# Kernel optimization log

Measured on AMD Instinct MI355X. Metric: run time of the kernel, lower is better.

Reference implementation:

```python
import jax, jax.numpy as jnp
import numpy as np

N_NODES = 40000
N_EDGES = 640000
IN_FEATS = 128
HID = 64
# layer widths per GCN.__init__: in->h->2h->2h->h->h->h->1
DIMS = [IN_FEATS, HID, 2 * HID, 2 * HID, HID, HID, HID, 1]


def setup_inputs() -> dict:
    key = jax.random.key(0)
    ks = jax.random.split(key, 3 + 2 * 7)
    inp = {
        "in_feat": jax.random.normal(ks[0], (N_NODES, IN_FEATS), dtype=jnp.float32),
        "src": jax.random.randint(ks[1], (N_EDGES,), 0, N_NODES, dtype=jnp.int32),
        "dst": jax.random.randint(ks[2], (N_EDGES,), 0, N_NODES, dtype=jnp.int32),
    }
    # DGL GraphConv params: weight [in, out] (glorot), bias [out] (zeros; use small randn for a nontrivial baseline)
    for i in range(7):
        din, dout = DIMS[i], DIMS[i + 1]
        scale = jnp.sqrt(6.0 / (din + dout)).astype(jnp.float32)
        inp[f"W{i+1}"] = jax.random.uniform(ks[3 + 2 * i], (din, dout), jnp.float32, -scale, scale)
        inp[f"b{i+1}"] = 0.01 * jax.random.normal(ks[4 + 2 * i], (dout,), dtype=jnp.float32)
    return inp


def _graph_conv(x, W, b, src, dst, out_norm, in_norm, n_nodes):
    # DGL GraphConv, norm='both', allow_zero_in_degree=True:
    #   h = D_in^{-1/2} * A^T * (D_out^{-1/2} * x) @ W + b
    x = x * out_norm[:, None]
    if x.shape[1] > W.shape[1]:
        # mult W first to shrink message dim (mirrors DGL's heuristic; math-equivalent)
        x = x @ W
        h = jax.ops.segment_sum(x[src], dst, num_segments=n_nodes)
    else:
        h = jax.ops.segment_sum(x[src], dst, num_segments=n_nodes)
        h = h @ W
    return h * in_norm[:, None] + b


def reference(in_feat, src, dst, W1, b1, W2, b2, W3, b3, W4, b4, W5, b5, W6, b6, W7, b7):
    n = in_feat.shape[0]
    ones = jnp.ones((src.shape[0],), dtype=jnp.float32)
    out_deg = jax.ops.segment_sum(ones, src, num_segments=n)
    in_deg = jax.ops.segment_sum(ones, dst, num_segments=n)
    out_norm = jnp.where(out_deg > 0, jax.lax.rsqrt(jnp.maximum(out_deg, 1.0)), 0.0)
    in_norm = jnp.where(in_deg > 0, jax.lax.rsqrt(jnp.maximum(in_deg, 1.0)), 0.0)

    params = [(W1, b1), (W2, b2), (W3, b3), (W4, b4), (W5, b5), (W6, b6), (W7, b7)]
    h = in_feat
    for i, (W, b) in enumerate(params):
        h = _graph_conv(h, W, b, src, dst, out_norm, in_norm, n)
        if i < 6:
            h = jax.nn.relu(h)
    return h  # [N, 1]
```

## Files before the change

kernel.cpp:

```cpp
#include <hip/hip_runtime.h>
#include <hip/hip_bf16.h>


#define IN_F 128
#define NSLICE 60
#define SHB 13
#define NSHARD 5

typedef __attribute__((ext_vector_type(8))) short short8v;
typedef __attribute__((ext_vector_type(4))) float f32x4;
typedef __attribute__((ext_vector_type(8))) _Float16 half8v;

static __device__ __forceinline__ unsigned short f2bf(float x) {
    unsigned u = __builtin_bit_cast(unsigned, x);
    unsigned r = (u + 0x7FFFu + ((u >> 16) & 1u)) >> 16;
    return (unsigned short)r;
}
static __device__ __forceinline__ float bf2f(unsigned short h) {
    unsigned u = ((unsigned)h) << 16;
    return __builtin_bit_cast(float, u);
}


__global__ __launch_bounds__(256) void hist2_kernel(const int* __restrict__ src,
                                                    const int* __restrict__ dst,
                                                    int* __restrict__ scratch, int E) {
    constexpr int SH = 1 << SHB;
    __shared__ int h[SH];
    const int t = threadIdx.x;
    const int b = blockIdx.x;
    const int s = blockIdx.y;
    const int z = blockIdx.z;
    const int* idx = z ? dst : src;
    for (int i = t; i < SH; i += 256) h[i] = 0;
    __syncthreads();
    const int per = (E + NSLICE - 1) / NSLICE;
    const int lo = b * per;
    const int hiE = min(lo + per, E);
    const int base = s << SHB;
    for (int e = lo + t; e < hiE; e += 256) {
        unsigned a = (unsigned)(idx[e] - base);
        if (a < (unsigned)SH) atomicAdd(&h[a], 1);
    }
    __syncthreads();
    int* so = scratch + ((size_t)((z * NSHARD + s) * NSLICE + b) << SHB);
    for (int i = t; i < SH; i += 256) so[i] = h[i];
}

__global__ void hist_reduce_kernel(const int* __restrict__ scratch,
                                   int* __restrict__ in_deg,
                                   float* __restrict__ out_nrm,
                                   float* __restrict__ in_nrm, int N) {
    constexpr int SH = 1 << SHB;
    int n = blockIdx.x * blockDim.x + threadIdx.x;
    if (n >= N) return;
    int s = n >> SHB;
    int i = n & (SH - 1);
    int od = 0, idg = 0;
    for (int b = 0; b < NSLICE; ++b) {
        od  += scratch[((size_t)((0 * NSHARD + s) * NSLICE + b) << SHB) + i];
        idg += scratch[((size_t)((1 * NSHARD + s) * NSLICE + b) << SHB) + i];
    }
    in_deg[n] = idg;
    out_nrm[n] = od  > 0 ? rsqrtf((float)od)  : 0.f;
    in_nrm[n]  = idg > 0 ? rsqrtf((float)idg) : 0.f;
}


__global__ __launch_bounds__(256) void scan_blk_kernel(const int* __restrict__ deg,
                                                       int* __restrict__ blockSums, int N) {
    __shared__ int ws[4];
    const int t = threadIdx.x;
    const int base = blockIdx.x * 1024 + t * 4;
    int4 v = make_int4(0, 0, 0, 0);
    if (base + 3 < N) v = *reinterpret_cast<const int4*>(&deg[base]);
    else if (base < N) {
        v.x = deg[base];
        if (base + 1 < N) v.y = deg[base + 1];
        if (base + 2 < N) v.z = deg[base + 2];
    }
    int s = v.x + v.y + v.z + v.w;
#pragma unroll
    for (int off = 32; off > 0; off >>= 1) s += __shfl_down(s, off);
    if ((t & 63) == 0) ws[t >> 6] = s;
    __syncthreads();
    if (t == 0) blockSums[blockIdx.x] = ws[0] + ws[1] + ws[2] + ws[3];
}

__global__ __launch_bounds__(64) void scan_top_kernel(const int* __restrict__ blockSums,
                                                      int* __restrict__ blockOffs,
                                                      int* __restrict__ row_off, int NB, int N) {
    const int t = threadIdx.x;
    int orig = (t < NB) ? blockSums[t] : 0;
    int v = orig;
#pragma unroll
    for (int off = 1; off < 64; off <<= 1) {
        int u = __shfl_up(v, off);
        if (t >= off) v += u;
    }
    if (t < NB) blockOffs[t] = v - orig;
    if (t == 63) row_off[N] = v;
}

__global__ __launch_bounds__(256) void scan_fill_kernel(const int* __restrict__ deg,
                                                        const int* __restrict__ blockOffs,
                                                        int* __restrict__ row_off,
                                                        int* __restrict__ cursor, int N) {
    __shared__ int wtot[4];
    const int t = threadIdx.x;
    const int lane = t & 63;
    const int wid = t >> 6;
    const int base = blockIdx.x * 1024 + t * 4;
    int4 v = make_int4(0, 0, 0, 0);
    if (base + 3 < N) v = *reinterpret_cast<const int4*>(&deg[base]);
    else if (base < N) {
        v.x = deg[base];
        if (base + 1 < N) v.y = deg[base + 1];
        if (base + 2 < N) v.z = deg[base + 2];
    }
    const int s = v.x + v.y + v.z + v.w;
    int incl = s;
#pragma unroll
    for (int off = 1; off < 64; off <<= 1) {
        int u = __shfl_up(incl, off);
        if (lane >= off) incl += u;
    }
    if (lane == 63) wtot[wid] = incl;
    __syncthreads();
    int pre = blockOffs[blockIdx.x] + incl - s;
    for (int i = 0; i < wid; ++i) pre += wtot[i];
    if (base < N) {
        int run = pre;
        row_off[base] = run; cursor[base] = run; run += v.x;
        if (base + 1 < N) { row_off[base + 1] = run; cursor[base + 1] = run; run += v.y; }
        if (base + 2 < N) { row_off[base + 2] = run; cursor[base + 2] = run; run += v.z; }
        if (base + 3 < N) { row_off[base + 3] = run; cursor[base + 3] = run; }
    }
}

__global__ void fill_kernel(const int* __restrict__ src, const int* __restrict__ dst,
                            int* __restrict__ cursor, int* __restrict__ csr, int E) {
    int e = blockIdx.x * blockDim.x + threadIdx.x;
    if (e < E) {
        int pos = atomicAdd(&cursor[dst[e]], 1);
        csr[pos] = src[e];
    }
}


__global__ void split_feat_kernel(const float* __restrict__ x, const float* __restrict__ snrm,
                                  unsigned short* __restrict__ th, unsigned short* __restrict__ tl,
                                  int total4) {
    int i = blockIdx.x * blockDim.x + threadIdx.x;
    if (i >= total4) return;
    float4 v = reinterpret_cast<const float4*>(x)[i];
    float sc = snrm[i >> 5];
    ushort4 h, l;
    float a;
    a = v.x * sc; h.x = f2bf(a); l.x = f2bf(a - bf2f(h.x));
    a = v.y * sc; h.y = f2bf(a); l.y = f2bf(a - bf2f(h.y));
    a = v.z * sc; h.z = f2bf(a); l.z = f2bf(a - bf2f(h.z));
    a = v.w * sc; h.w = f2bf(a); l.w = f2bf(a - bf2f(h.w));
    reinterpret_cast<ushort4*>(th)[i] = h;
    reinterpret_cast<ushort4*>(tl)[i] = l;
}

struct WDesc { const float* w; unsigned short* th; unsigned short* tl; int K; int N; };
struct WPack { WDesc d[6]; };

__global__ void split_w_kernel(WPack p) {
    WDesc d = p.d[blockIdx.x];
    int total = d.K * d.N;
    for (int i = threadIdx.x; i < total; i += blockDim.x) {
        int k = i / d.N, n = i - k * d.N;
        float v = d.w[i];
        unsigned short h = f2bf(v);
        d.th[(size_t)n * d.K + k] = h;
        d.tl[(size_t)n * d.K + k] = f2bf(v - bf2f(h));
    }
}


template<int K, int NOUT, bool POST, bool RELU, bool POST2, int OUTM>
__global__ __launch_bounds__(256) void gemm_mfma(
    const unsigned short* __restrict__ Ah, const unsigned short* __restrict__ Al,
    const unsigned short* __restrict__ Bh, const unsigned short* __restrict__ Bl,
    const float* __restrict__ r_nrm, const float* __restrict__ s_nrm,
    const float* __restrict__ bias,
    _Float16* __restrict__ Y16, unsigned short* __restrict__ Yh,
    unsigned short* __restrict__ Yl, int M) {
    constexpr int NT = NOUT / 16;
    const int lane = threadIdx.x & 63;
    const int wv = threadIdx.x >> 6;
    const int r0 = blockIdx.x * 64 + wv * 16;
    const int arow = r0 + (lane & 15);
    const int kg = (lane >> 4) * 8;

    f32x4 acc[NT];
#pragma unroll
    for (int n = 0; n < NT; ++n) acc[n] = (f32x4){0.f, 0.f, 0.f, 0.f};

    for (int kk = 0; kk < K; kk += 32) {
        short8v a_h = *reinterpret_cast<const short8v*>(Ah + (size_t)arow * K + kk + kg);
        short8v a_l = *reinterpret_cast<const short8v*>(Al + (size_t)arow * K + kk + kg);
#pragma unroll
        for (int n = 0; n < NT; ++n) {
            int col = n * 16 + (lane & 15);
            short8v b_h = *reinterpret_cast<const short8v*>(Bh + (size_t)col * K + kk + kg);
            short8v b_l = *reinterpret_cast<const short8v*>(Bl + (size_t)col * K + kk + kg);
            acc[n] = __builtin_amdgcn_mfma_f32_16x16x32_bf16(a_h, b_h, acc[n], 0, 0, 0);
            acc[n] = __builtin_amdgcn_mfma_f32_16x16x32_bf16(a_h, b_l, acc[n], 0, 0, 0);
            acc[n] = __builtin_amdgcn_mfma_f32_16x16x32_bf16(a_l, b_h, acc[n], 0, 0, 0);
        }
    }

    const int c0 = lane & 15;
    const int rr = r0 + (lane >> 4) * 4;
#pragma unroll
    for (int n = 0; n < NT; ++n) {
        const int col = n * 16 + c0;
        const float bcol = POST ? bias[col] : 0.f;
#pragma unroll
        for (int j = 0; j < 4; ++j) {
            const int row = rr + j;
            float y = acc[n][j];
            if (POST) y = fmaf(y, r_nrm[row], bcol);
            if (RELU) y = fmaxf(y, 0.f);
            if (POST2) y *= s_nrm[row];
            if (OUTM == 0) {
                Y16[(size_t)row * NOUT + col] = (_Float16)y;
            } else {
                unsigned short h = f2bf(y);
                Yh[(size_t)row * NOUT + col] = h;
                Yl[(size_t)row * NOUT + col] = f2bf(y - bf2f(h));
            }
        }
    }
}


template<int F, bool POST, bool RELU, bool POST2, int OUTM>
__global__ __launch_bounds__(256) void agg_h16(
    const _Float16* __restrict__ X, const int* __restrict__ csr,
    const int* __restrict__ row_off, const float* __restrict__ r_nrm,
    const float* __restrict__ s_nrm, const float* __restrict__ bias,
    _Float16* __restrict__ Y16, unsigned short* __restrict__ Yh,
    unsigned short* __restrict__ Yl, int N) {
    constexpr int LPE = F / 8;
    constexpr int EPW = 64 / LPE;
    const int lane = threadIdx.x & 63;
    const int node = blockIdx.x * (blockDim.x >> 6) + (threadIdx.x >> 6);
    if (node >= N) return;
    const int g = lane / LPE;
    const int c = lane % LPE;
    const int lo = row_off[node];
    const int hi = row_off[node + 1];
    float acc[8];
#pragma unroll
    for (int j = 0; j < 8; ++j) acc[j] = 0.f;
    for (int e = lo + g; e < hi; e += EPW) {
        int s = csr[e];
        half8v x = *reinterpret_cast<const half8v*>(&X[(size_t)s * F + c * 8]);
#pragma unroll
        for (int j = 0; j < 8; ++j) acc[j] += (float)x[j];
    }
#pragma unroll
    for (int m = LPE; m < 64; m <<= 1) {
#pragma unroll
        for (int j = 0; j < 8; ++j) acc[j] += __shfl_xor(acc[j], m);
    }
    if (lane < LPE) {
        if (POST) {
            float rn = r_nrm[node];
#pragma unroll
            for (int j = 0; j < 8; ++j) acc[j] = fmaf(acc[j], rn, bias[lane * 8 + j]);
        }
        if (RELU) {
#pragma unroll
            for (int j = 0; j < 8; ++j) acc[j] = fmaxf(acc[j], 0.f);
        }
        if (POST2) {
            float sn = s_nrm[node];
#pragma unroll
            for (int j = 0; j < 8; ++j) acc[j] *= sn;
        }
        if (OUTM == 0) {
            half8v o;
#pragma unroll
            for (int j = 0; j < 8; ++j) o[j] = (_Float16)acc[j];
            *reinterpret_cast<half8v*>(&Y16[(size_t)node * F + lane * 8]) = o;
        } else {
            short8v h, l;
#pragma unroll
            for (int j = 0; j < 8; ++j) {
                unsigned short hh = f2bf(acc[j]);
                h[j] = (short)hh;
                l[j] = (short)f2bf(acc[j] - bf2f(hh));
            }
            *reinterpret_cast<short8v*>(&Yh[(size_t)node * F + lane * 8]) = h;
            *reinterpret_cast<short8v*>(&Yl[(size_t)node * F + lane * 8]) = l;
        }
    }
}


__global__ __launch_bounds__(256) void gemv64_kernel(const _Float16* __restrict__ X,
                                                     const float* __restrict__ W,
                                                     float* __restrict__ Y, int M) {
    const int lane = threadIdx.x & 63;
    const int m = blockIdx.x * (blockDim.x >> 6) + (threadIdx.x >> 6);
    if (m >= M) return;
    float v = (float)X[(size_t)m * 64 + lane] * W[lane];
#pragma unroll
    for (int off = 32; off > 0; off >>= 1) v += __shfl_down(v, off);
    if (lane == 0) Y[m] = v;
}

__global__ __launch_bounds__(256) void agg1_kernel(const float* __restrict__ T,
                                                   const int* __restrict__ csr,
                                                   const int* __restrict__ row_off,
                                                   const float* __restrict__ r_nrm,
                                                   const float* __restrict__ bias,
                                                   float* __restrict__ Y, int N) {
    const int node = blockIdx.x * 16 + (threadIdx.x >> 4);
    const int l = threadIdx.x & 15;
    if (node >= N) return;
    const int lo = row_off[node];
    const int hi = row_off[node + 1];
    float acc = 0.f;
    for (int e = lo + l; e < hi; e += 16) acc += T[csr[e]];
#pragma unroll
    for (int m = 8; m >= 1; m >>= 1) acc += __shfl_xor(acc, m);
    if (l == 0) Y[node] = fmaf(acc, r_nrm[node], bias[0]);
}


extern "C" void kernel_launch(void* const* d_in, const int* in_sizes, int n_in,
                              void* d_out, int out_size, void* d_ws, size_t ws_size,
                              hipStream_t stream) {
    const float* in_feat = (const float*)d_in[0];
    const int* src = (const int*)d_in[1];
    const int* dst = (const int*)d_in[2];
    const float* W1 = (const float*)d_in[3];  const float* B1 = (const float*)d_in[4];
    const float* W2 = (const float*)d_in[5];  const float* B2 = (const float*)d_in[6];
    const float* W3 = (const float*)d_in[7];  const float* B3 = (const float*)d_in[8];
    const float* W4 = (const float*)d_in[9];  const float* B4 = (const float*)d_in[10];
    const float* W5 = (const float*)d_in[11]; const float* B5 = (const float*)d_in[12];
    const float* W6 = (const float*)d_in[13]; const float* B6 = (const float*)d_in[14];
    const float* W7 = (const float*)d_in[15]; const float* B7 = (const float*)d_in[16];

    const int N = in_sizes[0] / IN_F;
    const int E = in_sizes[1];
    float* out = (float*)d_out;

    char* w = (char*)d_ws;
    auto alloc = [&](size_t bytes) { char* p = w; w += (bytes + 255) & ~(size_t)255; return p; };
    int* csr      = (int*)alloc((size_t)E * 4);
    int* row_off  = (int*)alloc((size_t)(N + 1) * 4);
    int* cursor   = (int*)alloc((size_t)N * 4);
    int* in_deg   = (int*)alloc((size_t)N * 4);
    int* blockSums= (int*)alloc(64 * 4);
    int* blockOffs= (int*)alloc(64 * 4);
    float* out_nrm= (float*)alloc((size_t)N * 4);
    float* in_nrm = (float*)alloc((size_t)N * 4);
    float* t7     = (float*)alloc((size_t)N * 4);
    const int dims[8] = {128, 64, 128, 128, 64, 64, 64, 1};
    unsigned short* wth[6]; unsigned short* wtl[6];
    for (int i = 0; i < 6; ++i) {
        size_t kn = (size_t)dims[i] * dims[i + 1];
        wth[i] = (unsigned short*)alloc(kn * 2);
        wtl[i] = (unsigned short*)alloc(kn * 2);
    }
    unsigned short* fh = (unsigned short*)alloc((size_t)N * 128 * 2);
    unsigned short* fl = (unsigned short*)alloc((size_t)N * 128 * 2);
    unsigned short* th = (unsigned short*)alloc((size_t)N * 128 * 2);
    unsigned short* tl = (unsigned short*)alloc((size_t)N * 128 * 2);
    _Float16* h0 = (_Float16*)alloc((size_t)N * 128 * 2);
    _Float16* h1 = (_Float16*)alloc((size_t)N * 128 * 2);
    int* scratch = (int*)fh;
    (void)ws_size; (void)n_in; (void)out_size;

    const int TB = 256;
    const int NB = (N + 1023) / 1024;

    WPack wp;
    const float* Ws[6] = {W1, W2, W3, W4, W5, W6};
    for (int i = 0; i < 6; ++i) wp.d[i] = {Ws[i], wth[i], wtl[i], dims[i], dims[i + 1]};
    split_w_kernel<<<6, TB, 0, stream>>>(wp);

    hist2_kernel<<<dim3(NSLICE, NSHARD, 2), TB, 0, stream>>>(src, dst, scratch, E);
    hist_reduce_kernel<<<(N + TB - 1) / TB, TB, 0, stream>>>(
        scratch, in_deg, out_nrm, in_nrm, N);
    scan_blk_kernel<<<NB, TB, 0, stream>>>(in_deg, blockSums, N);
    scan_top_kernel<<<1, 64, 0, stream>>>(blockSums, blockOffs, row_off, NB, N);
    scan_fill_kernel<<<NB, TB, 0, stream>>>(in_deg, blockOffs, row_off, cursor, N);
    fill_kernel<<<(E + TB - 1) / TB, TB, 0, stream>>>(src, dst, cursor, csr, E);

    split_feat_kernel<<<(N * 32 + TB - 1) / TB, TB, 0, stream>>>(
        in_feat, out_nrm, fh, fl, N * 32);

    const int gridN4 = (N + 3) / 4;
    const int MB = N / 64;

    gemm_mfma<128, 64, false, false, false, 0><<<MB, TB, 0, stream>>>(
        fh, fl, wth[0], wtl[0], nullptr, nullptr, nullptr, h0, nullptr, nullptr, N);
    agg_h16<64, true, true, true, 0><<<gridN4, TB, 0, stream>>>(
        h0, csr, row_off, in_nrm, out_nrm, B1, h1, nullptr, nullptr, N);

    agg_h16<64, false, false, false, 1><<<gridN4, TB, 0, stream>>>(
        h1, csr, row_off, nullptr, nullptr, nullptr, nullptr, th, tl, N);
    gemm_mfma<64, 128, true, true, true, 0><<<MB, TB, 0, stream>>>(
        th, tl, wth[1], wtl[1], in_nrm, out_nrm, B2, h0, nullptr, nullptr, N);

    agg_h16<128, false, false, false, 1><<<gridN4, TB, 0, stream>>>(
        h0, csr, row_off, nullptr, nullptr, nullptr, nullptr, th, tl, N);
    gemm_mfma<128, 128, true, true, true, 1><<<MB, TB, 0, stream>>>(
        th, tl, wth[2], wtl[2], in_nrm, out_nrm, B3, nullptr, fh, fl, N);

    gemm_mfma<128, 64, false, false, false, 0><<<MB, TB, 0, stream>>>(
        fh, fl, wth[3], wtl[3], nullptr, nullptr, nullptr, h0, nullptr, nullptr, N);
    agg_h16<64, true, true, true, 0><<<gridN4, TB, 0, stream>>>(
        h0, csr, row_off, in_nrm, out_nrm, B4, h1, nullptr, nullptr, N);

    agg_h16<64, false, false, false, 1><<<gridN4, TB, 0, stream>>>(
        h1, csr, row_off, nullptr, nullptr, nullptr, nullptr, th, tl, N);
    gemm_mfma<64, 64, true, true, true, 0><<<MB, TB, 0, stream>>>(
        th, tl, wth[4], wtl[4], in_nrm, out_nrm, B5, h0, nullptr, nullptr, N);

    agg_h16<64, false, false, false, 1><<<gridN4, TB, 0, stream>>>(
        h0, csr, row_off, nullptr, nullptr, nullptr, nullptr, th, tl, N);
    gemm_mfma<64, 64, true, true, true, 0><<<MB, TB, 0, stream>>>(
        th, tl, wth[5], wtl[5], in_nrm, out_nrm, B6, h1, nullptr, nullptr, N);

    gemv64_kernel<<<gridN4, TB, 0, stream>>>(h1, W7, t7, N);
    agg1_kernel<<<(N + 15) / 16, TB, 0, stream>>>(t7, csr, row_off, in_nrm, B7, out, N);
}
```

Measured before the change: 343.8 us.

## Build CSR with per-slice LDS cursors from histogram; unroll aggregation; parallelize weight split

Result: faster. 310.2 us (-9.8%).

```diff
diff --git a/kernel.cpp b/kernel.cpp
--- a/kernel.cpp
+++ b/kernel.cpp
@@ -104,8 +104,7 @@
 
 __global__ __launch_bounds__(256) void scan_fill_kernel(const int* __restrict__ deg,
                                                         const int* __restrict__ blockOffs,
-                                                        int* __restrict__ row_off,
-                                                        int* __restrict__ cursor, int N) {
+                                                        int* __restrict__ row_off, int N) {
     __shared__ int wtot[4];
     const int t = threadIdx.x;
     const int lane = t & 63;
@@ -131,19 +130,51 @@
     for (int i = 0; i < wid; ++i) pre += wtot[i];
     if (base < N) {
         int run = pre;
-        row_off[base] = run; cursor[base] = run; run += v.x;
-        if (base + 1 < N) { row_off[base + 1] = run; cursor[base + 1] = run; run += v.y; }
-        if (base + 2 < N) { row_off[base + 2] = run; cursor[base + 2] = run; run += v.z; }
-        if (base + 3 < N) { row_off[base + 3] = run; cursor[base + 3] = run; }
-    }
-}
-
-__global__ void fill_kernel(const int* __restrict__ src, const int* __restrict__ dst,
-                            int* __restrict__ cursor, int* __restrict__ csr, int E) {
-    int e = blockIdx.x * blockDim.x + threadIdx.x;
-    if (e < E) {
-        int pos = atomicAdd(&cursor[dst[e]], 1);
-        csr[pos] = src[e];
+        row_off[base] = run; run += v.x;
+        if (base + 1 < N) { row_off[base + 1] = run; run += v.y; }
+        if (base + 2 < N) { row_off[base + 2] = run; run += v.z; }
+        if (base + 3 < N) { row_off[base + 3] = run; }
+    }
+}
+
+__global__ void slice_base_kernel(int* __restrict__ scratch,
+                                  const int* __restrict__ row_off, int N) {
+    constexpr int SH = 1 << SHB;
+    int n = blockIdx.x * blockDim.x + threadIdx.x;
+    if (n >= N) return;
+    int s = n >> SHB;
+    int i = n & (SH - 1);
+    int run = row_off[n];
+    for (int b = 0; b < NSLICE; ++b) {
+        size_t off = ((size_t)((NSHARD + s) * NSLICE + b) << SHB) + i;
+        int c = scratch[off];
+        scratch[off] = run;
+        run += c;
+    }
+}
+
+__global__ __launch_bounds__(256) void fill2_kernel(const int* __restrict__ src,
+                                                    const int* __restrict__ dst,
+                                                    const int* __restrict__ scratch,
+                                                    int* __restrict__ csr, int E) {
+    constexpr int SH = 1 << SHB;
+    __shared__ int cur[SH];
+    const int t = threadIdx.x;
+    const int b = blockIdx.x;
+    const int s = blockIdx.y;
+    const int* base = scratch + ((size_t)((NSHARD + s) * NSLICE + b) << SHB);
+    for (int i = t; i < SH; i += 256) cur[i] = base[i];
+    __syncthreads();
+    const int per = (E + NSLICE - 1) / NSLICE;
+    const int lo = b * per;
+    const int hiE = min(lo + per, E);
+    const int nb = s << SHB;
+    for (int e = lo + t; e < hiE; e += 256) {
+        unsigned a = (unsigned)(dst[e] - nb);
+        if (a < (unsigned)SH) {
+            int pos = atomicAdd(&cur[a], 1);
+            csr[pos] = src[e];
+        }
     }
 }
 
@@ -168,16 +199,15 @@
 struct WDesc { const float* w; unsigned short* th; unsigned short* tl; int K; int N; };
 struct WPack { WDesc d[6]; };
 
-__global__ void split_w_kernel(WPack p) {
+__global__ __launch_bounds__(256) void split_w_kernel(WPack p) {
     WDesc d = p.d[blockIdx.x];
-    int total = d.K * d.N;
-    for (int i = threadIdx.x; i < total; i += blockDim.x) {
-        int k = i / d.N, n = i - k * d.N;
-        float v = d.w[i];
-        unsigned short h = f2bf(v);
-        d.th[(size_t)n * d.K + k] = h;
-        d.tl[(size_t)n * d.K + k] = f2bf(v - bf2f(h));
-    }
+    int i = blockIdx.y * 256 + threadIdx.x;
+    if (i >= d.K * d.N) return;
+    int k = i / d.N, n = i - k * d.N;
+    float v = d.w[i];
+    unsigned short h = f2bf(v);
+    d.th[(size_t)n * d.K + k] = h;
+    d.tl[(size_t)n * d.K + k] = f2bf(v - bf2f(h));
 }
 
 
@@ -255,15 +285,26 @@
     const int c = lane % LPE;
     const int lo = row_off[node];
     const int hi = row_off[node + 1];
-    float acc[8];
-#pragma unroll
-    for (int j = 0; j < 8; ++j) acc[j] = 0.f;
-    for (int e = lo + g; e < hi; e += EPW) {
-        int s = csr[e];
-        half8v x = *reinterpret_cast<const half8v*>(&X[(size_t)s * F + c * 8]);
-#pragma unroll
-        for (int j = 0; j < 8; ++j) acc[j] += (float)x[j];
-    }
+    float acc[8], acc2[8];
+#pragma unroll
+    for (int j = 0; j < 8; ++j) { acc[j] = 0.f; acc2[j] = 0.f; }
+    int e = lo + g;
+    for (; e + EPW < hi; e += 2 * EPW) {
+        int s0 = csr[e];
+        int s1 = csr[e + EPW];
+        half8v x0 = *reinterpret_cast<const half8v*>(&X[(size_t)s0 * F + c * 8]);
+        half8v x1 = *reinterpret_cast<const half8v*>(&X[(size_t)s1 * F + c * 8]);
+#pragma unroll
+        for (int j = 0; j < 8; ++j) { acc[j] += (float)x0[j]; acc2[j] += (float)x1[j]; }
+    }
+    if (e < hi) {
+        int s0 = csr[e];
+        half8v x0 = *reinterpret_cast<const half8v*>(&X[(size_t)s0 * F + c * 8]);
+#pragma unroll
+        for (int j = 0; j < 8; ++j) acc[j] += (float)x0[j];
+    }
+#pragma unroll
+    for (int j = 0; j < 8; ++j) acc[j] += acc2[j];
 #pragma unroll
     for (int m = LPE; m < 64; m <<= 1) {
 #pragma unroll
@@ -357,7 +398,6 @@
     auto alloc = [&](size_t bytes) { char* p = w; w += (bytes + 255) & ~(size_t)255; return p; };
     int* csr      = (int*)alloc((size_t)E * 4);
     int* row_off  = (int*)alloc((size_t)(N + 1) * 4);
-    int* cursor   = (int*)alloc((size_t)N * 4);
     int* in_deg   = (int*)alloc((size_t)N * 4);
     int* blockSums= (int*)alloc(64 * 4);
     int* blockOffs= (int*)alloc(64 * 4);
@@ -386,15 +426,16 @@
     WPack wp;
     const float* Ws[6] = {W1, W2, W3, W4, W5, W6};
     for (int i = 0; i < 6; ++i) wp.d[i] = {Ws[i], wth[i], wtl[i], dims[i], dims[i + 1]};
-    split_w_kernel<<<6, TB, 0, stream>>>(wp);
+    split_w_kernel<<<dim3(6, 64), TB, 0, stream>>>(wp);
 
     hist2_kernel<<<dim3(NSLICE, NSHARD, 2), TB, 0, stream>>>(src, dst, scratch, E);
     hist_reduce_kernel<<<(N + TB - 1) / TB, TB, 0, stream>>>(
         scratch, in_deg, out_nrm, in_nrm, N);
     scan_blk_kernel<<<NB, TB, 0, stream>>>(in_deg, blockSums, N);
     scan_top_kernel<<<1, 64, 0, stream>>>(blockSums, blockOffs, row_off, NB, N);
-    scan_fill_kernel<<<NB, TB, 0, stream>>>(in_deg, blockOffs, row_off, cursor, N);
-    fill_kernel<<<(E + TB - 1) / TB, TB, 0, stream>>>(src, dst, cursor, csr, E);
+    scan_fill_kernel<<<NB, TB, 0, stream>>>(in_deg, blockOffs, row_off, N);
+    slice_base_kernel<<<(N + TB - 1) / TB, TB, 0, stream>>>(scratch, row_off, N);
+    fill2_kernel<<<dim3(NSLICE, NSHARD), TB, 0, stream>>>(src, dst, scratch, csr, E);
 
     split_feat_kernel<<<(N * 32 + TB - 1) / TB, TB, 0, stream>>>(
         in_feat, out_nrm, fh, fl, N * 32);
```
